# Optimization experiments

Hardware: AMD Instinct MI355X
Metric: run time of the kernel (lower is better)

## Reference

```python
import jax, jax.numpy as jnp
import numpy as np


def setup_inputs() -> dict:
    key = jax.random.key(0)
    ks = jax.random.split(key, 5)
    T, C_IN, C_OUT, H = 1024, 4, 2, 32
    x = jax.random.normal(ks[0], (T, C_IN), dtype=jnp.float32)
    # timestamps (relative positions); arange normalized to [0,1)
    t = jnp.arange(T, dtype=jnp.float32) / T
    # KernelNet params: Linear(3,H) -> Sine -> Linear(H,1)
    w1 = jax.random.normal(ks[1], (H, 3), dtype=jnp.float32) * (1.0 / np.sqrt(3.0))
    b1 = jax.random.normal(ks[2], (H,), dtype=jnp.float32) * 0.1
    w2 = jax.random.normal(ks[3], (1, H), dtype=jnp.float32) * (1.0 / np.sqrt(H))
    b2 = jax.random.normal(ks[4], (1,), dtype=jnp.float32) * 0.1
    return {"x": x, "t": t, "w1": w1, "b1": b1, "w2": w2, "b2": b2,
            "out_channels": C_OUT}


def reference(x, t, w1, b1, w2, b2, out_channels):
    # x: [T, C_in], t: [T]
    T, C_in = x.shape
    # dt[i, j] = t[j] - t[i]  (rep_t - rep_t.t() in the original)
    dt = t[None, :] - t[:, None]                                  # [T, T]
    # Kernel MLP input is [dt, in_channel_idx, out_channel_idx]; the first
    # Linear layer is affine, so split contributions: dt*w1[:,0] varies over
    # (i, j) while the channel-index part varies only over (o, c).
    h_dt = dt[:, :, None] * w1[:, 0]                              # [T, T, H]
    c_idx = jnp.arange(C_in, dtype=x.dtype)                       # [C_in]
    o_idx = jnp.arange(out_channels, dtype=x.dtype)               # [C_out]
    off = (o_idx[:, None, None] * w1[:, 2]
           + c_idx[None, :, None] * w1[:, 1]
           + b1)                                                  # [O, C, H]
    h = jnp.sin(h_dt[None, None] + off[:, :, None, None, :])      # [O, C, T, T, H]
    kernel = jnp.einsum('ocijh,h->ocij', h, w2[0]) + b2[0]        # [O, C, T, T]
    # causal mask: keep entries with j <= i (lower triangular), tiled per (o, c)
    mask = jnp.tril(jnp.ones((T, T), dtype=x.dtype))
    kernel = kernel * mask
    # y[i, o] = sum_{c, j<=i} kernel[o, c, i, j] * x[j, c]
    return jnp.einsum('ocij,jc->io', kernel, x)                   # [T, O]
```

## Files before the change

### kernel.cpp

```cpp
#include <hip/hip_runtime.h>
#include <math.h>

__global__ void ck_build_kernel_table(const float* __restrict__ t,
                                      const float* __restrict__ w1,
                                      const float* __restrict__ b1,
                                      const float* __restrict__ w2,
                                      const float* __restrict__ b2,
                                      float* __restrict__ Kt,
                                      int T, int Cin, int Cout, int H) {
    int idx = blockIdx.x * blockDim.x + threadIdx.x;
    int total = T * Cout * Cin;
    if (idx >= total) return;
    int oc  = Cout * Cin;
    int d   = idx / oc;
    int rem = idx - d * oc;
    int o   = rem / Cin;
    int c   = rem - o * Cin;

    float dt = t[0] - t[d];
    float fo = (float)o;
    float fc = (float)c;

    float acc = 0.0f;
    for (int h = 0; h < H; ++h) {
        float a = dt * w1[h * 3 + 0] + fc * w1[h * 3 + 1] + fo * w1[h * 3 + 2] + b1[h];
        acc += w2[h] * sinf(a);
    }
    Kt[idx] = acc + b2[0];
}

__global__ __launch_bounds__(256) void ck_causal_conv(
        const float* __restrict__ x,
        const float* __restrict__ Kt,
        float* __restrict__ out,
        int T) {
    const int i = blockIdx.x;
    float acc0 = 0.0f, acc1 = 0.0f;

    for (int j = threadIdx.x; j <= i; j += 256) {
        const int d = i - j;
        const float4 xv = *reinterpret_cast<const float4*>(x + j * 4);
        const float4 k0 = *reinterpret_cast<const float4*>(Kt + d * 8);
        const float4 k1 = *reinterpret_cast<const float4*>(Kt + d * 8 + 4);
        acc0 += k0.x * xv.x + k0.y * xv.y + k0.z * xv.z + k0.w * xv.w;
        acc1 += k1.x * xv.x + k1.y * xv.y + k1.z * xv.z + k1.w * xv.w;
    }

    #pragma unroll
    for (int off = 32; off > 0; off >>= 1) {
        acc0 += __shfl_down(acc0, off, 64);
        acc1 += __shfl_down(acc1, off, 64);
    }

    __shared__ float s0[4], s1[4];
    const int lane = threadIdx.x & 63;
    const int wid  = threadIdx.x >> 6;
    if (lane == 0) { s0[wid] = acc0; s1[wid] = acc1; }
    __syncthreads();
    if (threadIdx.x == 0) {
        float a = s0[0] + s0[1] + s0[2] + s0[3];
        float b = s1[0] + s1[1] + s1[2] + s1[3];
        out[i * 2 + 0] = a;
        out[i * 2 + 1] = b;
    }
}

extern "C" void kernel_launch(void* const* d_in, const int* in_sizes, int n_in,
                              void* d_out, int out_size, void* d_ws, size_t ws_size,
                              hipStream_t stream) {
    const float* x  = (const float*)d_in[0];
    const float* t  = (const float*)d_in[1];
    const float* w1 = (const float*)d_in[2];
    const float* b1 = (const float*)d_in[3];
    const float* w2 = (const float*)d_in[4];
    const float* b2 = (const float*)d_in[5];
    float* out = (float*)d_out;

    const int T    = in_sizes[1];
    const int Cin  = in_sizes[0] / T;
    const int H    = in_sizes[3];
    const int Cout = out_size / T;

    float* Kt = (float*)d_ws;

    const int total   = T * Cout * Cin;
    const int blocks1 = (total + 255) / 256;
    ck_build_kernel_table<<<blocks1, 256, 0, stream>>>(t, w1, b1, w2, b2, Kt,
                                                       T, Cin, Cout, H);
    ck_causal_conv<<<T, 256, 0, stream>>>(x, Kt, out, T);
}
```

Measured before the change: 75.07 us.

## Fuse kernel-table build and causal conv into one LDS-resident kernel

```diff
diff --git a/kernel.cpp b/kernel.cpp
--- a/kernel.cpp
+++ b/kernel.cpp
@@ -1,5 +1,96 @@
 #include <hip/hip_runtime.h>
 #include <math.h>
+
+
+__global__ __launch_bounds__(512) void ck_fused(
+        const float* __restrict__ x,
+        const float* __restrict__ t,
+        const float* __restrict__ w1,
+        const float* __restrict__ b1,
+        const float* __restrict__ w2,
+        const float* __restrict__ b2,
+        float* __restrict__ out) {
+    __shared__ float Kt[8][1024];
+    __shared__ float xs[4][1024];
+    __shared__ float pq[32][16];
+    __shared__ float av[32];
+
+    const int tid = threadIdx.x;
+
+    #pragma unroll
+    for (int r = 0; r < 2; ++r) {
+        const int j = tid + r * 512;
+        const float4 xv = *reinterpret_cast<const float4*>(x + j * 4);
+        xs[0][j] = xv.x; xs[1][j] = xv.y; xs[2][j] = xv.z; xs[3][j] = xv.w;
+    }
+
+    if (tid < 256) {
+        const int och = tid >> 5;
+        const int h   = tid & 31;
+        const int o = och >> 2, c = och & 3;
+        const float v  = (float)c * w1[h * 3 + 1] + (float)o * w1[h * 3 + 2] + b1[h];
+        const float wh = w2[h];
+        pq[h][och]     = wh * cosf(v);
+        pq[h][och + 8] = wh * sinf(v);
+        if (och == 0) av[h] = w1[h * 3 + 0];
+    }
+    __syncthreads();
+
+    {
+        const float t0  = t[0];
+        const float dt0 = t0 - t[tid];
+        const float dt1 = t0 - t[tid + 512];
+        float acc0[8], acc1[8];
+        #pragma unroll
+        for (int k = 0; k < 8; ++k) { acc0[k] = 0.0f; acc1[k] = 0.0f; }
+
+        for (int h = 0; h < 32; ++h) {
+            const float a   = av[h];
+            const float4 P0 = *reinterpret_cast<const float4*>(&pq[h][0]);
+            const float4 P1 = *reinterpret_cast<const float4*>(&pq[h][4]);
+            const float4 Q0 = *reinterpret_cast<const float4*>(&pq[h][8]);
+            const float4 Q1 = *reinterpret_cast<const float4*>(&pq[h][12]);
+            const float u0 = dt0 * a, u1 = dt1 * a;
+            const float s0 = __sinf(u0), c0 = __cosf(u0);
+            const float s1 = __sinf(u1), c1 = __cosf(u1);
+            const float p[8] = {P0.x, P0.y, P0.z, P0.w, P1.x, P1.y, P1.z, P1.w};
+            const float q[8] = {Q0.x, Q0.y, Q0.z, Q0.w, Q1.x, Q1.y, Q1.z, Q1.w};
+            #pragma unroll
+            for (int k = 0; k < 8; ++k) {
+                acc0[k] = fmaf(s0, p[k], fmaf(c0, q[k], acc0[k]));
+                acc1[k] = fmaf(s1, p[k], fmaf(c1, q[k], acc1[k]));
+            }
+        }
+        const float b2v = b2[0];
+        #pragma unroll
+        for (int k = 0; k < 8; ++k) {
+            Kt[k][tid]       = acc0[k] + b2v;
+            Kt[k][tid + 512] = acc1[k] + b2v;
+        }
+    }
+    __syncthreads();
+
+    const int wv = tid >> 6;
+    const int ln = tid & 63;
+    const int i  = (blockIdx.x << 3) + wv;
+    float y0 = 0.0f, y1 = 0.0f;
+    for (int j = ln; j <= i; j += 64) {
+        const int d = i - j;
+        const float x0 = xs[0][j], x1 = xs[1][j], x2 = xs[2][j], x3 = xs[3][j];
+        y0 += Kt[0][d] * x0 + Kt[1][d] * x1 + Kt[2][d] * x2 + Kt[3][d] * x3;
+        y1 += Kt[4][d] * x0 + Kt[5][d] * x1 + Kt[6][d] * x2 + Kt[7][d] * x3;
+    }
+    #pragma unroll
+    for (int off = 32; off > 0; off >>= 1) {
+        y0 += __shfl_down(y0, off, 64);
+        y1 += __shfl_down(y1, off, 64);
+    }
+    if (ln == 0) {
+        out[i * 2 + 0] = y0;
+        out[i * 2 + 1] = y1;
+    }
+}
+
 
 __global__ void ck_build_kernel_table(const float* __restrict__ t,
                                       const float* __restrict__ w1,
@@ -81,11 +172,14 @@
     const int H    = in_sizes[3];
     const int Cout = out_size / T;
 
-    float* Kt = (float*)d_ws;
-
-    const int total   = T * Cout * Cin;
-    const int blocks1 = (total + 255) / 256;
-    ck_build_kernel_table<<<blocks1, 256, 0, stream>>>(t, w1, b1, w2, b2, Kt,
-                                                       T, Cin, Cout, H);
-    ck_causal_conv<<<T, 256, 0, stream>>>(x, Kt, out, T);
+    if (T == 1024 && Cin == 4 && Cout == 2 && H == 32) {
+        ck_fused<<<128, 512, 0, stream>>>(x, t, w1, b1, w2, b2, out);
+    } else {
+        float* Kt = (float*)d_ws;
+        const int total   = T * Cout * Cin;
+        const int blocks1 = (total + 255) / 256;
+        ck_build_kernel_table<<<blocks1, 256, 0, stream>>>(t, w1, b1, w2, b2, Kt,
+                                                           T, Cin, Cout, H);
+        ck_causal_conv<<<T, 256, 0, stream>>>(x, Kt, out, T);
+    }
 }
```

After: 71.90 us. 1.04x faster.
